# Kernel optimization log

Hardware: AMD Instinct MI355X
Metric: run time of the kernel (lower is better)

## Reference

```python
import jax, jax.numpy as jnp
import numpy as np

N_NODES = 50000
N_EDGES = 400000
IN_FEAT = 1024
HID = 128
HEADS = 2
N_Z = 32
NEG_SLOPE = 0.2


def _glorot(key, shape):
    fan_in, fan_out = shape[0], shape[-1]
    s = jnp.sqrt(6.0 / (fan_in + fan_out)).astype(jnp.float32)
    return jax.random.uniform(key, shape, jnp.float32, -s, s)


def setup_inputs() -> dict:
    key = jax.random.key(0)
    ks = jax.random.split(key, 20)
    x = jax.random.normal(ks[0], (N_NODES, IN_FEAT), jnp.float32)
    edge_index = jax.random.randint(ks[1], (2, N_EDGES), 0, N_NODES, dtype=jnp.int64)
    d = {"x": x, "edge_index": edge_index}
    # layer dims: (in, heads, out_per_head)
    dims = [(IN_FEAT, HEADS, HID), (HEADS * HID, HEADS, HID), (HEADS * HID, HEADS, HID), (HEADS * HID, 1, N_Z)]
    ki = 2
    for li, (fin, h, c) in enumerate(dims):
        d[f"Wl{li}"] = _glorot(ks[ki], (fin, h * c)); ki += 1
        d[f"Wr{li}"] = _glorot(ks[ki], (fin, h * c)); ki += 1
        d[f"att{li}"] = _glorot(ks[ki], (h, c)); ki += 1
        d[f"b{li}"] = jnp.zeros((h * c,), jnp.float32)
    return d


def gatv2_layer(x, src, dst, Wl, Wr, att, bias, concat):
    """GATv2Conv (PyG defaults: share_weights=False, negative_slope=0.2)."""
    N = x.shape[0]
    H, C = att.shape
    xl = (x @ Wl).reshape(N, H, C)  # source transform
    xr = (x @ Wr).reshape(N, H, C)  # target transform
    e = jax.nn.leaky_relu(xl[src] + xr[dst], NEG_SLOPE)       # [E,H,C]
    logits = jnp.einsum('ehc,hc->eh', e, att)                 # [E,H]
    # segment softmax over incoming edges of each dst node
    m = jax.ops.segment_max(logits, dst, num_segments=N)      # [N,H]
    p = jnp.exp(logits - m[dst])
    denom = jax.ops.segment_sum(p, dst, num_segments=N)
    alpha = p / denom[dst]                                    # [E,H]
    out = jax.ops.segment_sum(alpha[:, :, None] * xl[src], dst, num_segments=N)  # [N,H,C]
    out = out.reshape(N, H * C) if concat else out.mean(axis=1)
    return out + bias


def reference(x, edge_index, Wl0, Wr0, att0, b0, Wl1, Wr1, att1, b1,
              Wl2, Wr2, att2, b2, Wl3, Wr3, att3, b3):
    N = x.shape[0]
    loop = jnp.arange(N, dtype=edge_index.dtype)
    src = jnp.concatenate([edge_index[0], loop])  # add self loops (PyG default)
    dst = jnp.concatenate([edge_index[1], loop])
    h = gatv2_layer(x, src, dst, Wl0, Wr0, att0, b0, True)
    h = gatv2_layer(h, src, dst, Wl1, Wr1, att1, b1, True)
    h = gatv2_layer(h, src, dst, Wl2, Wr2, att2, b2, True)
    h = gatv2_layer(h, src, dst, Wl3, Wr3, att3, b3, True)  # heads=1: concat == identity
    return h  # [N, n_z] ; ext_emb is None so forward returns h directly
```

## Files before the change

### kernel.cpp

```cpp
#include <hip/hip_runtime.h>
#include <math.h>

#define NEG_SLOPE 0.2f

typedef __attribute__((ext_vector_type(8))) short bf16x8;
typedef __attribute__((ext_vector_type(4))) float f32x4;

__device__ __forceinline__ float b2f(unsigned short u) {
    return __uint_as_float(((unsigned)u) << 16);
}
__device__ __forceinline__ unsigned short f2b(float f) {
    unsigned u = __float_as_uint(f);
    unsigned r = (u + 0x7fffu + ((u >> 16) & 1u)) >> 16;
    return (unsigned short)r;
}

__device__ __forceinline__ void async_copy16(const void* g, void* l) {
    __builtin_amdgcn_global_load_lds(
        (const __attribute__((address_space(1))) void*)g,
        (__attribute__((address_space(3))) void*)l, 16, 0, 0);
}

__global__ __launch_bounds__(256) void gemm_bf16(
    const unsigned short* __restrict__ A,
    const unsigned short* __restrict__ Bt,
    unsigned short* __restrict__ C,
    int M, int K, int Nc)
{
    __shared__ unsigned short As[128 * 32];
    __shared__ unsigned short Bs[128 * 32];
    const int tid = threadIdx.x;
    const int w = tid >> 6, lane = tid & 63;
    const int tm = blockIdx.x * 128;
    const int tn = blockIdx.y * 128;

    const int off0 = w * 64 + lane;
    const int row0 = off0 >> 2, q0 = off0 & 3;
    const int qg0 = q0 ^ ((row0 >> 1) & 3);
    const int off1 = 256 + w * 64 + lane;
    const int row1 = off1 >> 2, q1 = off1 & 3;
    const int qg1 = q1 ^ ((row1 >> 1) & 3);

    const int ar0 = min(tm + row0, M - 1), ar1 = min(tm + row1, M - 1);
    const int bn0 = min(tn + row0, Nc - 1), bn1 = min(tn + row1, Nc - 1);
    const unsigned short* pa0 = A + (size_t)ar0 * K + qg0 * 8;
    const unsigned short* pa1 = A + (size_t)ar1 * K + qg1 * 8;
    const unsigned short* pb0 = Bt + (size_t)bn0 * K + qg0 * 8;
    const unsigned short* pb1 = Bt + (size_t)bn1 * K + qg1 * 8;
    unsigned short* lA0 = As + (size_t)(w * 64) * 8;
    unsigned short* lA1 = As + (size_t)(256 + w * 64) * 8;
    unsigned short* lB0 = Bs + (size_t)(w * 64) * 8;
    unsigned short* lB1 = Bs + (size_t)(256 + w * 64) * 8;

    const int m0 = (w & 1) * 64, n0 = (w >> 1) * 64;
    const int fr = lane & 15, Q = lane >> 4;
    const unsigned short* aptr[4];
    const unsigned short* bptr[4];
    #pragma unroll
    for (int i = 0; i < 4; ++i) {
        int ra = m0 + i * 16 + fr;
        aptr[i] = As + (ra * 64 + ((Q ^ ((ra >> 1) & 3)) * 16)) / 2;
        int rb = n0 + i * 16 + fr;
        bptr[i] = Bs + (rb * 64 + ((Q ^ ((rb >> 1) & 3)) * 16)) / 2;
    }

    f32x4 acc[4][4] = {};
    for (int kk = 0; kk < K; kk += 32) {
        async_copy16(pa0 + kk, lA0);
        async_copy16(pa1 + kk, lA1);
        async_copy16(pb0 + kk, lB0);
        async_copy16(pb1 + kk, lB1);
        __syncthreads();
        bf16x8 af[4], bfr[4];
        #pragma unroll
        for (int i = 0; i < 4; ++i) {
            af[i]  = *(const bf16x8*)aptr[i];
            bfr[i] = *(const bf16x8*)bptr[i];
        }
        #pragma unroll
        for (int mi = 0; mi < 4; ++mi)
            #pragma unroll
            for (int ni = 0; ni < 4; ++ni)
                acc[mi][ni] = __builtin_amdgcn_mfma_f32_16x16x32_bf16(
                    af[mi], bfr[ni], acc[mi][ni], 0, 0, 0);
        __syncthreads();
    }

    #pragma unroll
    for (int mi = 0; mi < 4; ++mi) {
        #pragma unroll
        for (int ni = 0; ni < 4; ++ni) {
            int col = tn + n0 + ni * 16 + fr;
            #pragma unroll
            for (int r = 0; r < 4; ++r) {
                int row = tm + m0 + mi * 16 + Q * 4 + r;
                if (row < M && col < Nc)
                    C[(size_t)row * Nc + col] = f2b(acc[mi][ni][r]);
            }
        }
    }
}

__global__ __launch_bounds__(256) void cvt_f2b_degzero(
    const float* __restrict__ in, unsigned short* __restrict__ outp,
    int total4, int* __restrict__ deg, int n)
{
    int i = blockIdx.x * 256 + threadIdx.x;
    if (i < n) deg[i] = 0;
    if (i >= total4) return;
    float4 v = ((const float4*)in)[i];
    ushort4 o = make_ushort4(f2b(v.x), f2b(v.y), f2b(v.z), f2b(v.w));
    ((ushort4*)outp)[i] = o;
}

__global__ __launch_bounds__(256) void cvt_wt_all(
    const float* __restrict__ Wl0, const float* __restrict__ Wr0,
    const float* __restrict__ Wl1, const float* __restrict__ Wr1,
    const float* __restrict__ Wl2, const float* __restrict__ Wr2,
    const float* __restrict__ Wl3, const float* __restrict__ Wr3,
    unsigned short* __restrict__ WT)
{
    int id = blockIdx.x * 256 + threadIdx.x;
    const float *Wl, *Wr; int fin, HC, local; unsigned short* dst;
    if (id < 524288)      { Wl = Wl0; Wr = Wr0; fin = 1024; HC = 256; dst = WT;          local = id; }
    else if (id < 655360) { Wl = Wl1; Wr = Wr1; fin = 256;  HC = 256; dst = WT + 524288; local = id - 524288; }
    else if (id < 786432) { Wl = Wl2; Wr = Wr2; fin = 256;  HC = 256; dst = WT + 655360; local = id - 655360; }
    else if (id < 802816) { Wl = Wl3; Wr = Wr3; fin = 256;  HC = 32;  dst = WT + 786432; local = id - 786432; }
    else return;
    int n = local / fin, k = local - n * fin;
    float v = (n < HC) ? Wl[(size_t)k * HC + n] : Wr[(size_t)k * HC + (n - HC)];
    dst[local] = f2b(v);
}

__global__ __launch_bounds__(256) void deg_count(
    const int* __restrict__ ei, int* __restrict__ deg, int E0, int E)
{
    int e = blockIdx.x * 256 + threadIdx.x;
    if (e >= E) return;
    int d = (e < E0) ? ei[E0 + e] : e - E0;
    atomicAdd(deg + d, 1);
}

__global__ __launch_bounds__(256) void scan_blocks(
    const int* __restrict__ deg, int* __restrict__ rp,
    int* __restrict__ bsums, int n)
{
    __shared__ int sm[256];
    int base = blockIdx.x * 1024;
    int t = threadIdx.x;
    int i0 = base + t * 4;
    int v0 = (i0 + 0 < n) ? deg[i0 + 0] : 0;
    int v1 = (i0 + 1 < n) ? deg[i0 + 1] : 0;
    int v2 = (i0 + 2 < n) ? deg[i0 + 2] : 0;
    int v3 = (i0 + 3 < n) ? deg[i0 + 3] : 0;
    int tsum = v0 + v1 + v2 + v3;
    sm[t] = tsum;
    __syncthreads();
    for (int off = 1; off < 256; off <<= 1) {
        int val = (t >= off) ? sm[t - off] : 0;
        __syncthreads();
        sm[t] += val;
        __syncthreads();
    }
    int exb = sm[t] - tsum;
    if (t == 255) bsums[blockIdx.x] = sm[255];
    if (i0 + 0 < n) rp[i0 + 0] = exb;
    if (i0 + 1 < n) rp[i0 + 1] = exb + v0;
    if (i0 + 2 < n) rp[i0 + 2] = exb + v0 + v1;
    if (i0 + 3 < n) rp[i0 + 3] = exb + v0 + v1 + v2;
}

__global__ void scan_bsums(int* __restrict__ bsums, int nb)
{
    __shared__ int sm[64];
    int t = threadIdx.x;
    int v = (t < nb) ? bsums[t] : 0;
    sm[t] = v;
    __syncthreads();
    for (int off = 1; off < 64; off <<= 1) {
        int val = (t >= off) ? sm[t - off] : 0;
        __syncthreads();
        sm[t] += val;
        __syncthreads();
    }
    if (t < nb) bsums[t] = sm[t] - v;
}

__global__ __launch_bounds__(256) void scan_finalize(
    int* __restrict__ rp, int* __restrict__ cur,
    const int* __restrict__ bsums, int n)
{
    int i = blockIdx.x * 256 + threadIdx.x;
    if (i < n) {
        int v = rp[i] + bsums[i >> 10];
        rp[i] = v;
        cur[i] = v;
    }
}

__global__ __launch_bounds__(256) void csr_fill(
    const int* __restrict__ ei, int* __restrict__ cur,
    int* __restrict__ csrc, int E0, int E)
{
    int e = blockIdx.x * 256 + threadIdx.x;
    if (e >= E) return;
    int s, d;
    if (e < E0) { s = ei[e]; d = ei[E0 + e]; } else { s = e - E0; d = s; }
    int pos = atomicAdd(cur + d, 1);
    csrc[pos] = s;
}

template<int T, int STRIDE, int SHW>
__device__ __forceinline__ void gat_chunk(
    const unsigned short* __restrict__ xlr, const int* __restrict__ cp,
    int laneoff, float bx, float by, float bz, float bw, float4 wv,
    float& m, float& l, float4& acc)
{
    int idx[T];
    #pragma unroll
    for (int t = 0; t < T; ++t) idx[t] = cp[t];
    ushort4 rb[T];
    #pragma unroll
    for (int t = 0; t < T; ++t)
        rb[t] = *(const ushort4*)(xlr + (size_t)idx[t] * STRIDE + laneoff);
    #pragma unroll
    for (int t = 0; t < T; ++t) {
        float ax = b2f(rb[t].x), ay = b2f(rb[t].y);
        float az = b2f(rb[t].z), aw = b2f(rb[t].w);
        float y, dot = 0.f;
        y = ax + bx; y = (y > 0.f) ? y : NEG_SLOPE * y; dot += y * wv.x;
        y = ay + by; y = (y > 0.f) ? y : NEG_SLOPE * y; dot += y * wv.y;
        y = az + bz; y = (y > 0.f) ? y : NEG_SLOPE * y; dot += y * wv.z;
        y = aw + bw; y = (y > 0.f) ? y : NEG_SLOPE * y; dot += y * wv.w;
        #pragma unroll
        for (int mk = 1; mk < SHW; mk <<= 1) dot += __shfl_xor(dot, mk, 64);
        float mn = fmaxf(m, dot);
        float scale = __expf(m - mn);
        float p = __expf(dot - mn);
        l = l * scale + p;
        acc.x = acc.x * scale + p * ax;
        acc.y = acc.y * scale + p * ay;
        acc.z = acc.z * scale + p * az;
        acc.w = acc.w * scale + p * aw;
        m = mn;
    }
}

__global__ __launch_bounds__(256) void aggr_csr_256(
    const unsigned short* __restrict__ xlr,
    const float* __restrict__ att, const float* __restrict__ bias,
    const int* __restrict__ csrc, const int* __restrict__ rp,
    const int* __restrict__ deg, unsigned short* __restrict__ outb, int N)
{
    int node = blockIdx.x * 4 + (threadIdx.x >> 6);
    if (node >= N) return;
    int lane = threadIdx.x & 63;
    int laneoff = lane * 4;
    ushort4 bu = *(const ushort4*)(xlr + (size_t)node * 512 + 256 + laneoff);
    float bx = b2f(bu.x), by = b2f(bu.y), bz = b2f(bu.z), bw = b2f(bu.w);
    float4 wv = *(const float4*)(att + laneoff);
    int start = rp[node];
    int g = deg[node];
    const int* cp = csrc + start;
    float m = -INFINITY, l = 0.f;
    float4 acc = make_float4(0.f, 0.f, 0.f, 0.f);
    int j = 0;
    while (j + 8 <= g) {
        gat_chunk<8, 512, 32>(xlr, cp + j, laneoff, bx, by, bz, bw, wv, m, l, acc);
        j += 8;
    }
    if (j + 4 <= g) {
        gat_chunk<4, 512, 32>(xlr, cp + j, laneoff, bx, by, bz, bw, wv, m, l, acc);
        j += 4;
    }
    if (j + 2 <= g) {
        gat_chunk<2, 512, 32>(xlr, cp + j, laneoff, bx, by, bz, bw, wv, m, l, acc);
        j += 2;
    }
    if (j < g) {
        gat_chunk<1, 512, 32>(xlr, cp + j, laneoff, bx, by, bz, bw, wv, m, l, acc);
    }
    float inv = 1.f / l;
    float4 bi = *(const float4*)(bias + laneoff);
    ushort4 o = make_ushort4(f2b(acc.x * inv + bi.x), f2b(acc.y * inv + bi.y),
                             f2b(acc.z * inv + bi.z), f2b(acc.w * inv + bi.w));
    *(ushort4*)(outb + (size_t)node * 256 + laneoff) = o;
}

__global__ __launch_bounds__(256) void aggr_csr_32(
    const unsigned short* __restrict__ xlr,
    const float* __restrict__ att, const float* __restrict__ bias,
    const int* __restrict__ csrc, const int* __restrict__ rp,
    const int* __restrict__ deg, float* __restrict__ out, int N)
{
    int node = blockIdx.x * 32 + (threadIdx.x >> 3);
    if (node >= N) return;
    int lane8 = threadIdx.x & 7;
    int laneoff = lane8 * 4;
    ushort4 bu = *(const ushort4*)(xlr + (size_t)node * 64 + 32 + laneoff);
    float bx = b2f(bu.x), by = b2f(bu.y), bz = b2f(bu.z), bw = b2f(bu.w);
    float4 wv = *(const float4*)(att + laneoff);
    int start = rp[node];
    int g = deg[node];
    const int* cp = csrc + start;
    float m = -INFINITY, l = 0.f;
    float4 acc = make_float4(0.f, 0.f, 0.f, 0.f);
    int j = 0;
    while (j + 8 <= g) {
        gat_chunk<8, 64, 8>(xlr, cp + j, laneoff, bx, by, bz, bw, wv, m, l, acc);
        j += 8;
    }
    if (j + 4 <= g) {
        gat_chunk<4, 64, 8>(xlr, cp + j, laneoff, bx, by, bz, bw, wv, m, l, acc);
        j += 4;
    }
    if (j + 2 <= g) {
        gat_chunk<2, 64, 8>(xlr, cp + j, laneoff, bx, by, bz, bw, wv, m, l, acc);
        j += 2;
    }
    if (j < g) {
        gat_chunk<1, 64, 8>(xlr, cp + j, laneoff, bx, by, bz, bw, wv, m, l, acc);
    }
    float inv = 1.f / l;
    float4 bi = *(const float4*)(bias + laneoff);
    float4 o;
    o.x = acc.x * inv + bi.x;
    o.y = acc.y * inv + bi.y;
    o.z = acc.z * inv + bi.z;
    o.w = acc.w * inv + bi.w;
    *(float4*)(out + (size_t)node * 32 + laneoff) = o;
}

extern "C" void kernel_launch(void* const* d_in, const int* in_sizes, int n_in,
                              void* d_out, int out_size, void* d_ws, size_t ws_size,
                              hipStream_t stream)
{
    const float* x  = (const float*)d_in[0];
    const int*   ei = (const int*)d_in[1];
    const float* Wl[4]   = {(const float*)d_in[2], (const float*)d_in[6], (const float*)d_in[10], (const float*)d_in[14]};
    const float* Wr[4]   = {(const float*)d_in[3], (const float*)d_in[7], (const float*)d_in[11], (const float*)d_in[15]};
    const float* attw[4] = {(const float*)d_in[4], (const float*)d_in[8], (const float*)d_in[12], (const float*)d_in[16]};
    const float* bias[4] = {(const float*)d_in[5], (const float*)d_in[9], (const float*)d_in[13], (const float*)d_in[17]};
    float* outp = (float*)d_out;

    const int N  = in_sizes[0] / 1024;
    const int E0 = in_sizes[1] / 2;
    const int E  = E0 + N;
    const int NB = (N + 1023) / 1024;

    int* deg   = (int*)d_ws;
    int* rp    = deg + N;
    int* cur   = rp + N;
    int* bsums = cur + N;
    int* csrc  = bsums + 64;
    unsigned short* WT  = (unsigned short*)(csrc + E);
    unsigned short* xb  = WT + 802816;
    unsigned short* hb  = xb;
    unsigned short* xlr = xb + (size_t)N * 1024;
    const int wtOff[4] = {0, 524288, 655360, 786432};

    dim3 blk(256);

    cvt_f2b_degzero<<<((size_t)N * 1024 / 4 + 255) / 256, blk, 0, stream>>>(
        x, xb, N * 1024 / 4, deg, N);
    deg_count<<<(E + 255) / 256, blk, 0, stream>>>(ei, deg, E0, E);
    scan_blocks<<<NB, blk, 0, stream>>>(deg, rp, bsums, N);
    scan_bsums<<<1, 64, 0, stream>>>(bsums, NB);
    scan_finalize<<<(N + 255) / 256, blk, 0, stream>>>(rp, cur, bsums, N);
    csr_fill<<<(E + 255) / 256, blk, 0, stream>>>(ei, cur, csrc, E0, E);
    cvt_wt_all<<<(802816 + 255) / 256, blk, 0, stream>>>(
        Wl[0], Wr[0], Wl[1], Wr[1], Wl[2], Wr[2], Wl[3], Wr[3], WT);

    const int gm = (N + 127) / 128;
    for (int l = 0; l < 4; ++l) {
        const int HC  = (l == 3) ? 32 : 256;
        const int fin = (l == 0) ? 1024 : 256;
        const int Nc  = 2 * HC;
        const unsigned short* Ain = (l == 0) ? xb : hb;

        gemm_bf16<<<dim3(gm, (Nc + 127) / 128), blk, 0, stream>>>(
            Ain, WT + wtOff[l], xlr, N, fin, Nc);

        if (l < 3) {
            aggr_csr_256<<<(N + 3) / 4, blk, 0, stream>>>(
                xlr, attw[l], bias[l], csrc, rp, deg, hb, N);
        } else {
            aggr_csr_32<<<(N + 31) / 32, blk, 0, stream>>>(
                xlr, attw[l], bias[l], csrc, rp, deg, outp, N);
        }
    }
}
```

Before: 751.7 us.

## Remap GEMM blocks per XCD and widen aggregation lanes to 8 features

The GEMM launch becomes a 1D grid whose block index is remapped so that consecutive blocks, which the hardware spreads round-robin across the 8 XCDs, handle all N-tiles of the same M rows on one XCD. This is meant to improve L2 reuse of the A rows. The 256-wide aggregation kernel now gives each node half a wavefront (32 lanes) with 16-byte loads of 8 bf16 features per lane, packing 8 nodes per block. That means wider gathers and a shorter shuffle reduction, at the cost of more registers per lane.

Result: faster. 706.0 us (-6.1%).

```diff
diff --git a/kernel.cpp b/kernel.cpp
--- a/kernel.cpp
+++ b/kernel.cpp
@@ -5,6 +5,7 @@
 
 typedef __attribute__((ext_vector_type(8))) short bf16x8;
 typedef __attribute__((ext_vector_type(4))) float f32x4;
+typedef __attribute__((ext_vector_type(8))) unsigned short u16x8;
 
 __device__ __forceinline__ float b2f(unsigned short u) {
     return __uint_as_float(((unsigned)u) << 16);
@@ -25,14 +26,19 @@
     const unsigned short* __restrict__ A,
     const unsigned short* __restrict__ Bt,
     unsigned short* __restrict__ C,
-    int M, int K, int Nc)
+    int M, int K, int Nc, int gm, int gn)
 {
     __shared__ unsigned short As[128 * 32];
     __shared__ unsigned short Bs[128 * 32];
+    const int b = blockIdx.x;
+    const int xcd = b & 7, grp = b >> 3;
+    const int nb = grp % gn, mbl = grp / gn;
+    const int mb = mbl * 8 + xcd;
+    if (mb >= gm) return;
+    const int tm = mb * 128;
+    const int tn = nb * 128;
     const int tid = threadIdx.x;
     const int w = tid >> 6, lane = tid & 63;
-    const int tm = blockIdx.x * 128;
-    const int tn = blockIdx.y * 128;
 
     const int off0 = w * 64 + lane;
     const int row0 = off0 >> 2, q0 = off0 & 3;
@@ -210,6 +216,77 @@
     csrc[pos] = s;
 }
 
+template<int T>
+__device__ __forceinline__ void gat_chunk8(
+    const unsigned short* __restrict__ xlr, const int* __restrict__ cp,
+    int fo, const float* bx, const float* wv,
+    float& m, float& l, float* acc)
+{
+    int idx[T];
+    #pragma unroll
+    for (int t = 0; t < T; ++t) idx[t] = cp[t];
+    u16x8 rb[T];
+    #pragma unroll
+    for (int t = 0; t < T; ++t)
+        rb[t] = *(const u16x8*)(xlr + (size_t)idx[t] * 512 + fo);
+    #pragma unroll
+    for (int t = 0; t < T; ++t) {
+        float a[8];
+        #pragma unroll
+        for (int i = 0; i < 8; ++i) a[i] = b2f(rb[t][i]);
+        float dot = 0.f;
+        #pragma unroll
+        for (int i = 0; i < 8; ++i) {
+            float y = a[i] + bx[i];
+            y = (y > 0.f) ? y : NEG_SLOPE * y;
+            dot += y * wv[i];
+        }
+        #pragma unroll
+        for (int mk = 1; mk < 16; mk <<= 1) dot += __shfl_xor(dot, mk, 64);
+        float mn = fmaxf(m, dot);
+        float scale = __expf(m - mn);
+        float p = __expf(dot - mn);
+        l = l * scale + p;
+        #pragma unroll
+        for (int i = 0; i < 8; ++i) acc[i] = acc[i] * scale + p * a[i];
+        m = mn;
+    }
+}
+
+__global__ __launch_bounds__(256) void aggr_csr_256(
+    const unsigned short* __restrict__ xlr,
+    const float* __restrict__ att, const float* __restrict__ bias,
+    const int* __restrict__ csrc, const int* __restrict__ rp,
+    const int* __restrict__ deg, unsigned short* __restrict__ outb, int N)
+{
+    int node = blockIdx.x * 8 + (threadIdx.x >> 5);
+    if (node >= N) return;
+    int fo = (threadIdx.x & 31) * 8;
+    u16x8 bu = *(const u16x8*)(xlr + (size_t)node * 512 + 256 + fo);
+    float bx[8], wv[8], acc[8];
+    #pragma unroll
+    for (int i = 0; i < 8; ++i) { bx[i] = b2f(bu[i]); acc[i] = 0.f; }
+    *(float4*)(wv)     = *(const float4*)(att + fo);
+    *(float4*)(wv + 4) = *(const float4*)(att + fo + 4);
+    int start = rp[node];
+    int g = deg[node];
+    const int* cp = csrc + start;
+    float m = -INFINITY, l = 0.f;
+    int j = 0;
+    while (j + 8 <= g) { gat_chunk8<8>(xlr, cp + j, fo, bx, wv, m, l, acc); j += 8; }
+    if (j + 4 <= g)    { gat_chunk8<4>(xlr, cp + j, fo, bx, wv, m, l, acc); j += 4; }
+    if (j + 2 <= g)    { gat_chunk8<2>(xlr, cp + j, fo, bx, wv, m, l, acc); j += 2; }
+    if (j < g)         { gat_chunk8<1>(xlr, cp + j, fo, bx, wv, m, l, acc); }
+    float inv = 1.f / l;
+    float bi[8];
+    *(float4*)(bi)     = *(const float4*)(bias + fo);
+    *(float4*)(bi + 4) = *(const float4*)(bias + fo + 4);
+    u16x8 o;
+    #pragma unroll
+    for (int i = 0; i < 8; ++i) o[i] = f2b(acc[i] * inv + bi[i]);
+    *(u16x8*)(outb + (size_t)node * 256 + fo) = o;
+}
+
 template<int T, int STRIDE, int SHW>
 __device__ __forceinline__ void gat_chunk(
     const unsigned short* __restrict__ xlr, const int* __restrict__ cp,
@@ -244,47 +321,6 @@
         acc.w = acc.w * scale + p * aw;
         m = mn;
     }
-}
-
-__global__ __launch_bounds__(256) void aggr_csr_256(
-    const unsigned short* __restrict__ xlr,
-    const float* __restrict__ att, const float* __restrict__ bias,
-    const int* __restrict__ csrc, const int* __restrict__ rp,
-    const int* __restrict__ deg, unsigned short* __restrict__ outb, int N)
-{
-    int node = blockIdx.x * 4 + (threadIdx.x >> 6);
-    if (node >= N) return;
-    int lane = threadIdx.x & 63;
-    int laneoff = lane * 4;
-    ushort4 bu = *(const ushort4*)(xlr + (size_t)node * 512 + 256 + laneoff);
-    float bx = b2f(bu.x), by = b2f(bu.y), bz = b2f(bu.z), bw = b2f(bu.w);
-    float4 wv = *(const float4*)(att + laneoff);
-    int start = rp[node];
-    int g = deg[node];
-    const int* cp = csrc + start;
-    float m = -INFINITY, l = 0.f;
-    float4 acc = make_float4(0.f, 0.f, 0.f, 0.f);
-    int j = 0;
-    while (j + 8 <= g) {
-        gat_chunk<8, 512, 32>(xlr, cp + j, laneoff, bx, by, bz, bw, wv, m, l, acc);
-        j += 8;
-    }
-    if (j + 4 <= g) {
-        gat_chunk<4, 512, 32>(xlr, cp + j, laneoff, bx, by, bz, bw, wv, m, l, acc);
-        j += 4;
-    }
-    if (j + 2 <= g) {
-        gat_chunk<2, 512, 32>(xlr, cp + j, laneoff, bx, by, bz, bw, wv, m, l, acc);
-        j += 2;
-    }
-    if (j < g) {
-        gat_chunk<1, 512, 32>(xlr, cp + j, laneoff, bx, by, bz, bw, wv, m, l, acc);
-    }
-    float inv = 1.f / l;
-    float4 bi = *(const float4*)(bias + laneoff);
-    ushort4 o = make_ushort4(f2b(acc.x * inv + bi.x), f2b(acc.y * inv + bi.y),
-                             f2b(acc.z * inv + bi.z), f2b(acc.w * inv + bi.w));
-    *(ushort4*)(outb + (size_t)node * 256 + laneoff) = o;
 }
 
 __global__ __launch_bounds__(256) void aggr_csr_32(
@@ -372,17 +408,19 @@
         Wl[0], Wr[0], Wl[1], Wr[1], Wl[2], Wr[2], Wl[3], Wr[3], WT);
 
     const int gm = (N + 127) / 128;
+    const int gm8 = (gm + 7) / 8;
     for (int l = 0; l < 4; ++l) {
         const int HC  = (l == 3) ? 32 : 256;
         const int fin = (l == 0) ? 1024 : 256;
         const int Nc  = 2 * HC;
+        const int gn  = (Nc + 127) / 128;
         const unsigned short* Ain = (l == 0) ? xb : hb;
 
-        gemm_bf16<<<dim3(gm, (Nc + 127) / 128), blk, 0, stream>>>(
-            Ain, WT + wtOff[l], xlr, N, fin, Nc);
+        gemm_bf16<<<8 * gn * gm8, blk, 0, stream>>>(
+            Ain, WT + wtOff[l], xlr, N, fin, Nc, gm, gn);
 
         if (l < 3) {
-            aggr_csr_256<<<(N + 3) / 4, blk, 0, stream>>>(
+            aggr_csr_256<<<(N + 7) / 8, blk, 0, stream>>>(
                 xlr, attw[l], bias[l], csrc, rp, deg, hb, N);
         } else {
             aggr_csr_32<<<(N + 31) / 32, blk, 0, stream>>>(
```
